# Kernel tuning notes

Hardware: AMD Instinct MI355X
Metric: run time of the kernel (lower is better)

The kernel has to match this reference:

```python
import jax, jax.numpy as jnp
import numpy as np

B, N, COUT, CIN, H, W = 16, 4, 256, 256, 64, 64


def setup_inputs() -> dict:
    key = jax.random.key(0)
    k1, k2, k3, k4 = jax.random.split(key, 4)
    x = jax.random.normal(k1, (B, CIN, H, W), jnp.float32)
    alphas = jax.random.uniform(k2, (B, N), jnp.float32)          # routing weights (lambdas)
    angles = jax.random.normal(k3, (B, N), jnp.float32) * 0.5     # thetas, mixed signs
    # kaiming_normal_(mode='fan_out', relu): std = sqrt(2 / (Cout * k * k))
    std = np.sqrt(2.0 / (COUT * 9)).astype(np.float32)
    weight = jax.random.normal(k4, (N, COUT, CIN, 3, 3), jnp.float32) * std
    return {"x": x, "alphas": alphas, "angles": angles, "weight": weight}


def _rot_mats(thetas):
    """thetas: [M] -> rotation matrices [M, 9, 9] (row, col), matching torch builder."""
    xc = jnp.cos(thetas)
    ys = jnp.sin(thetas)
    a = xc - ys
    b = xc * ys
    c = xc + ys
    z = jnp.zeros_like(xc)
    o = jnp.ones_like(xc)

    def mat(rows):
        # rows: list of 9 lists of 9 [M]-arrays -> [M, 9, 9]
        return jnp.stack([jnp.stack(r, axis=-1) for r in rows], axis=-2)

    pos = mat([
        [a, 1 - a, z, z, z, z, z, z, z],
        [z, xc - b, b, z, 1 - c + b, ys - b, z, z, z],
        [z, z, a, z, z, 1 - a, z, z, z],
        [b, ys - b, z, xc - b, 1 - c + b, z, z, z, z],
        [z, z, z, z, o, z, z, z, z],
        [z, z, z, z, 1 - c + b, xc - b, z, ys - b, b],
        [z, z, z, 1 - a, z, z, a, z, z],
        [z, z, z, ys - b, 1 - c + b, z, b, xc - b, z],
        [z, z, z, z, z, z, z, 1 - a, a],
    ])
    neg = mat([
        [c, z, z, 1 - c, z, z, z, z, z],
        [-b, xc + b, z, b - ys, 1 - a - b, z, z, z, z],
        [z, 1 - c, c, z, z, z, z, z, z],
        [z, z, z, xc + b, 1 - a - b, z, -b, b - ys, z],
        [z, z, z, z, o, z, z, z, z],
        [z, b - ys, -b, z, 1 - a - b, xc + b, z, z, z],
        [z, z, z, z, z, z, c, 1 - c, z],
        [z, z, z, z, 1 - a - b, b - ys, z, xc + b, -b],
        [z, z, z, z, z, 1 - c, z, z, c],
    ])
    m = (thetas >= 0).astype(thetas.dtype)[:, None, None]
    return m * pos + (1 - m) * neg


def reference(x, alphas, angles, weight):
    bsz, Cin, h, w = x.shape
    n, Cout = weight.shape[0], weight.shape[1]
    # [bsz, n, 9, 9] rotation matrices scaled by routing lambdas
    rm = _rot_mats(angles.reshape(-1)).reshape(bsz, n, 9, 9)
    rm = rm * alphas[:, :, None, None]
    # weights [n, Cout, Cin, 3, 3] -> [n, 9, Cout*Cin]
    Wf = weight.transpose(0, 3, 4, 1, 2).reshape(n, 9, Cout * Cin)
    # mix over kernel_number n and source tap q -> per-sample rotated kernels
    rw = jnp.einsum('bnpq,nqm->bpm', rm, Wf)          # [bsz, 9, Cout*Cin]
    rw = rw.reshape(bsz, 3, 3, Cout, Cin).transpose(0, 3, 4, 1, 2)
    rw = rw.reshape(bsz * Cout, Cin, 3, 3)
    # per-sample conv via grouped conv on flattened batch
    xr = x.reshape(1, bsz * Cin, h, w)
    out = jax.lax.conv_general_dilated(
        xr, rw, window_strides=(1, 1), padding=((1, 1), (1, 1)),
        dimension_numbers=('NCHW', 'OIHW', 'NCHW'), feature_group_count=bsz)
    return out.reshape(bsz, Cout, out.shape[2], out.shape[3])
```

## Files before the change

### kernel.cpp

```cpp
#include <hip/hip_runtime.h>
#include <hip/hip_bf16.h>

#define B_    16
#define N_    4
#define COUT  256
#define CIN   256
#define H_    64
#define W_    64
#define K_TOT (CIN * 9)
#define HW    (H_ * W_)
#define NKT   (K_TOT / 32)
#define PAD   66
#define PLANE (PAD * PAD)

typedef __attribute__((ext_vector_type(8))) short short8;
typedef __attribute__((ext_vector_type(4))) float f32x4;
typedef unsigned short ushort_t;

static __device__ __forceinline__ ushort_t f2bf(float f) {
    __hip_bfloat16 h = __float2bfloat16(f);
    return *reinterpret_cast<ushort_t*>(&h);
}

typedef __attribute__((address_space(3))) unsigned int lds_u32;
typedef __attribute__((address_space(1))) const unsigned int glb_u32;
static __device__ __forceinline__ void gl_lds16(const ushort_t* g, ushort_t* l) {
    __builtin_amdgcn_global_load_lds((glb_u32*)g, (lds_u32*)l, 16, 0, 0);
}

#define BARRIER() asm volatile("s_barrier" ::: "memory")
#define VMCNTN(N) asm volatile("s_waitcnt vmcnt(" #N ")" ::: "memory")

__global__ void rot_mats_kernel(const float* __restrict__ alphas,
                                const float* __restrict__ angles,
                                float* __restrict__ rm) {
    int i = threadIdx.x;
    if (i >= B_ * N_) return;
    float th = angles[i], al = alphas[i];
    float xc = cosf(th), ys = sinf(th);
    float a = xc - ys, b = xc * ys, c = xc + ys;
    float r[81];
#pragma unroll
    for (int j = 0; j < 81; ++j) r[j] = 0.f;
    if (th >= 0.f) {
        r[0] = a;          r[1] = 1.f - a;
        r[10] = xc - b;    r[11] = b;        r[13] = 1.f - c + b; r[14] = ys - b;
        r[20] = a;         r[23] = 1.f - a;
        r[27] = b;         r[28] = ys - b;   r[30] = xc - b;      r[31] = 1.f - c + b;
        r[40] = 1.f;
        r[49] = 1.f - c + b; r[50] = xc - b; r[52] = ys - b;      r[53] = b;
        r[57] = 1.f - a;   r[60] = a;
        r[66] = ys - b;    r[67] = 1.f - c + b; r[69] = b;        r[70] = xc - b;
        r[79] = 1.f - a;   r[80] = a;
    } else {
        r[0] = c;          r[3] = 1.f - c;
        r[9] = -b;         r[10] = xc + b;   r[12] = b - ys;      r[13] = 1.f - a - b;
        r[19] = 1.f - c;   r[20] = c;
        r[30] = xc + b;    r[31] = 1.f - a - b; r[33] = -b;       r[34] = b - ys;
        r[40] = 1.f;
        r[46] = b - ys;    r[47] = -b;       r[49] = 1.f - a - b; r[50] = xc + b;
        r[60] = c;         r[61] = 1.f - c;
        r[67] = 1.f - a - b; r[68] = b - ys; r[70] = xc + b;      r[71] = -b;
        r[77] = 1.f - c;   r[80] = c;
    }
#pragma unroll
    for (int j = 0; j < 81; ++j) rm[i * 81 + j] = r[j] * al;
}

__global__ __launch_bounds__(256)
void build_rw_kernel(const float* __restrict__ weight,
                     const float* __restrict__ rm,
                     ushort_t* __restrict__ rw) {
    __shared__ float rms[N_ * 81];
    int tid = threadIdx.x;
    int b = blockIdx.y;
    for (int j = tid; j < N_ * 81; j += 256)
        rms[j] = rm[b * N_ * 81 + j];
    __syncthreads();

    int idx = blockIdx.x * 256 + tid;
    int cout = idx >> 8, cin = idx & 255;

    float wv[N_][9];
#pragma unroll
    for (int n = 0; n < N_; ++n)
#pragma unroll
        for (int q = 0; q < 9; ++q)
            wv[n][q] = weight[(size_t)(n * (COUT * CIN) + idx) * 9 + q];

    ushort_t* dst = rw + (size_t)(b * COUT + cout) * K_TOT + cin;
#pragma unroll
    for (int p = 0; p < 9; ++p) {
        float s = 0.f;
#pragma unroll
        for (int n = 0; n < N_; ++n)
#pragma unroll
            for (int q = 0; q < 9; ++q)
                s += rms[n * 81 + p * 9 + q] * wv[n][q];
        dst[p * 256] = f2bf(s);
    }
}

__global__ __launch_bounds__(256)
void halo_zero_kernel(ushort_t* __restrict__ xt) {
    ushort_t* base = xt + (size_t)blockIdx.x * PLANE * 64;
    int t = threadIdx.x;
    for (int i = t; i < 260; i += 256) {
        int py, px;
        if (i < 66)       { py = 0;  px = i; }
        else if (i < 132) { py = 65; px = i - 66; }
        else if (i < 196) { py = i - 132 + 1; px = 0; }
        else              { py = i - 196 + 1; px = 65; }
        ushort_t* d = base + (size_t)(py * PAD + px) * 64;
        int4 z = {0, 0, 0, 0};
#pragma unroll
        for (int q = 0; q < 8; ++q) *(int4*)(d + q * 8) = z;
    }
}

__global__ __launch_bounds__(256)
void nhwc_kernel(const float* __restrict__ x, ushort_t* __restrict__ xt) {
    int y    = blockIdx.x;
    int cb32 = blockIdx.y;
    int b    = blockIdx.z;
    __shared__ ushort_t tileT[64][40];
    int t = threadIdx.x;

    int ci = t & 31, seg = t >> 5;
    const float* src = x + ((size_t)(b * CIN + cb32 * 32 + ci) * HW + y * 64 + seg * 8);
    float4 f0 = ((const float4*)src)[0];
    float4 f1 = ((const float4*)src)[1];
#pragma unroll
    for (int q = 0; q < 4; ++q) tileT[seg * 8 + q][ci]     = f2bf(((float*)&f0)[q]);
#pragma unroll
    for (int q = 0; q < 4; ++q) tileT[seg * 8 + 4 + q][ci] = f2bf(((float*)&f1)[q]);
    __syncthreads();

    int px = t >> 2, cseg = t & 3;
    ushort_t* dst = xt + ((size_t)(b * 4 + (cb32 >> 1)) * PLANE + (y + 1) * PAD + px + 1) * 64
                       + (cb32 & 1) * 32 + cseg * 8;
    *(int4*)dst = *(const int4*)&tileT[px][cseg * 8];
}

__global__ __launch_bounds__(512, 1)
void conv_kernel(const ushort_t* __restrict__ xt,
                 const ushort_t* __restrict__ rw,
                 float* __restrict__ out) {
    int bid0 = blockIdx.x;
    int bid = (bid0 & 7) * 32 + (bid0 >> 3);
    int b    = bid >> 4;
    int tile = bid & 15;
    int y0 = tile * 4;
    int tid = threadIdx.x;
    int lane = tid & 63, wid = tid >> 6;
    int wm = wid >> 2, wn = wid & 3;
    int rA = lane & 15, kseg = lane >> 4;

    __shared__ __align__(16) ushort_t As[4][256][32];
    __shared__ __align__(16) ushort_t Bs[4][256][32];
    ushort_t* AsB = &As[0][0][0];
    ushort_t* BsB = &Bs[0][0][0];

    f32x4 acc[8][4] = {};

    const ushort_t* rwb  = rw + (size_t)b * COUT * K_TOT;
    const ushort_t* xtb2 = xt + (size_t)b * 4 * PLANE * 64 + (size_t)y0 * PAD * 64;

    const int r0 = tid >> 2;
    const int sd = tid & 3;
    const int fs = (r0 & 3) ^ ((r0 >> 2) & 3);
    const int sg = (sd ^ fs) * 8;
    const int a0 = r0 * K_TOT + sg;
    const int a1 = (r0 + 128) * K_TOT + sg;
    const int pb0 = ((r0 >> 6) * PAD + (r0 & 63)) * 64 + sg;
    const int pb1 = pb0 + 2 * PAD * 64;
    const int dd0 = tid * 8;
    const int dd1 = 4096 + tid * 8;
    const int fread = (rA & 3) ^ ((rA >> 2) & 3);
    const int cread = (kseg ^ fread) * 8;

#define STAGE_A(KTN)                                                           \
    {                                                                          \
        int p_ = (KTN) >> 3, c32_ = (KTN) & 7;                                 \
        int ako = p_ * 256 + c32_ * 32;                                        \
        ushort_t* db = AsB + ((KTN) & 3) * 8192;                               \
        gl_lds16(rwb + a0 + ako, db + dd0);                                    \
        gl_lds16(rwb + a1 + ako, db + dd1);                                    \
    }

#define STAGE_B(KTN)                                                           \
    {                                                                          \
        int p_ = (KTN) >> 3, cb4_ = ((KTN) & 7) >> 1, h_ = (KTN) & 1;          \
        int ph_ = p_ / 3, pw_ = p_ - 3 * ph_;                                  \
        const ushort_t* sb = xtb2 + (size_t)(cb4_ * PLANE + ph_ * PAD + pw_) * 64 \
                             + h_ * 32;                                        \
        ushort_t* db = BsB + ((KTN) & 3) * 8192;                               \
        gl_lds16(sb + pb0, db + dd0);                                          \
        gl_lds16(sb + pb1, db + dd1);                                          \
    }

#define READ_AF(Q, MH2)                                                        \
    _Pragma("unroll")                                                          \
    for (int mi = 0; mi < 4; ++mi) {                                           \
        int row = wm * 128 + (MH2) * 64 + mi * 16 + rA;                        \
        af[mi] = *(const short8*)(AsB + (Q) * 8192 + row * 32 + cread);        \
    }

#define READ_BF(Q)                                                             \
    _Pragma("unroll")                                                          \
    for (int ni = 0; ni < 4; ++ni) {                                           \
        int row = wn * 64 + ni * 16 + rA;                                      \
        bf[ni] = *(const short8*)(BsB + (Q) * 8192 + row * 32 + cread);        \
    }

#define DO_MFMA(MH2)                                                           \
    __builtin_amdgcn_s_setprio(1);                                             \
    _Pragma("unroll")                                                          \
    for (int mi = 0; mi < 4; ++mi)                                             \
        _Pragma("unroll")                                                      \
        for (int ni = 0; ni < 4; ++ni)                                         \
            acc[(MH2) * 4 + mi][ni] = __builtin_amdgcn_mfma_f32_16x16x32_bf16( \
                af[mi], bf[ni], acc[(MH2) * 4 + mi][ni], 0, 0, 0);             \
    __builtin_amdgcn_s_setprio(0);

    STAGE_A(0); STAGE_B(0);
    STAGE_A(1); STAGE_B(1);
    STAGE_A(2); STAGE_B(2);
    VMCNTN(8);
    BARRIER();

    short8 af[4], bf[4];
    for (int kt = 0; kt < NKT; ++kt) {
        int q = kt & 3;
        bool more = (kt + 3 < NKT);
        READ_AF(q, 0);
        READ_BF(q);
        if (more) STAGE_A(kt + 3);
        BARRIER();
        DO_MFMA(0);
        BARRIER();
        READ_AF(q, 1);
        if (more) STAGE_B(kt + 3);
        BARRIER();
        DO_MFMA(1);
        if (kt < NKT - 3)       { VMCNTN(8); }
        else if (kt == NKT - 3) { VMCNTN(4); }
        else if (kt == NKT - 2) { VMCNTN(0); }
        BARRIER();
    }
#undef STAGE_A
#undef STAGE_B
#undef READ_AF
#undef READ_BF
#undef DO_MFMA

    int row0 = (lane >> 4) * 4;
    int col  = lane & 15;
    float* outb = out + (size_t)b * COUT * HW + tile * 256;
#pragma unroll
    for (int am = 0; am < 8; ++am)
#pragma unroll
        for (int an = 0; an < 4; ++an)
#pragma unroll
            for (int rr = 0; rr < 4; ++rr) {
                int m = wm * 128 + am * 16 + row0 + rr;
                int n = wn * 64 + an * 16 + col;
                outb[(size_t)m * HW + n] = acc[am][an][rr];
            }
}

extern "C" void kernel_launch(void* const* d_in, const int* in_sizes, int n_in,
                              void* d_out, int out_size, void* d_ws, size_t ws_size,
                              hipStream_t stream) {
    const float* x      = (const float*)d_in[0];
    const float* alphas = (const float*)d_in[1];
    const float* angles = (const float*)d_in[2];
    const float* weight = (const float*)d_in[3];
    float* out = (float*)d_out;

    ushort_t* rw = (ushort_t*)d_ws;
    ushort_t* xt = (ushort_t*)((char*)d_ws + (size_t)B_ * COUT * K_TOT * 2);
    float*    rm = (float*)((char*)d_ws + (size_t)B_ * COUT * K_TOT * 2
                                        + (size_t)64 * PLANE * 64 * 2);

    rot_mats_kernel<<<1, 64, 0, stream>>>(alphas, angles, rm);
    build_rw_kernel<<<dim3(COUT * CIN / 256, B_), 256, 0, stream>>>(weight, rm, rw);
    halo_zero_kernel<<<64, 256, 0, stream>>>(xt);
    nhwc_kernel<<<dim3(64, 8, B_), 256, 0, stream>>>(x, xt);
    conv_kernel<<<256, 512, 0, stream>>>(xt, rw, out);
}
```

Baseline: 124.6 us.

## Halve conv N-tile to 128 pixels, double K-step to 64, triple-buffer

The conv GEMM tile changes from 256x256 to 256x128 (two output rows per block), which doubles the grid to 512 blocks so more of the CUs are filled. The K step per iteration doubles to 64 with a new XOR swizzle over 8 chunks, and the LDS pipeline moves from four to three stages with A and B staged together. Halving the tile lowers accumulator register pressure and raises parallelism. In exchange, each block reloads the weight tile for half as many pixels, so global and L2 traffic for the A operand roughly doubles.

```diff
diff --git a/kernel.cpp b/kernel.cpp
--- a/kernel.cpp
+++ b/kernel.cpp
@@ -9,7 +9,7 @@
 #define W_    64
 #define K_TOT (CIN * 9)
 #define HW    (H_ * W_)
-#define NKT   (K_TOT / 32)
+#define NKT   (K_TOT / 64)
 #define PAD   66
 #define PLANE (PAD * PAD)
 
@@ -147,70 +147,74 @@
                  const ushort_t* __restrict__ rw,
                  float* __restrict__ out) {
     int bid0 = blockIdx.x;
-    int bid = (bid0 & 7) * 32 + (bid0 >> 3);
-    int b    = bid >> 4;
-    int tile = bid & 15;
-    int y0 = tile * 4;
+    int bid = (bid0 & 7) * 64 + (bid0 >> 3);
+    int b    = bid >> 5;
+    int tile = bid & 31;
+    int y0 = tile * 2;
     int tid = threadIdx.x;
     int lane = tid & 63, wid = tid >> 6;
     int wm = wid >> 2, wn = wid & 3;
     int rA = lane & 15, kseg = lane >> 4;
 
-    __shared__ __align__(16) ushort_t As[4][256][32];
-    __shared__ __align__(16) ushort_t Bs[4][256][32];
+    __shared__ __align__(16) ushort_t As[3][256][64];
+    __shared__ __align__(16) ushort_t Bs[3][128][64];
     ushort_t* AsB = &As[0][0][0];
     ushort_t* BsB = &Bs[0][0][0];
 
-    f32x4 acc[8][4] = {};
+    f32x4 acc[8][2] = {};
 
     const ushort_t* rwb  = rw + (size_t)b * COUT * K_TOT;
     const ushort_t* xtb2 = xt + (size_t)b * 4 * PLANE * 64 + (size_t)y0 * PAD * 64;
 
-    const int r0 = tid >> 2;
-    const int sd = tid & 3;
-    const int fs = (r0 & 3) ^ ((r0 >> 2) & 3);
-    const int sg = (sd ^ fs) * 8;
-    const int a0 = r0 * K_TOT + sg;
-    const int a1 = (r0 + 128) * K_TOT + sg;
-    const int pb0 = ((r0 >> 6) * PAD + (r0 & 63)) * 64 + sg;
-    const int pb1 = pb0 + 2 * PAD * 64;
-    const int dd0 = tid * 8;
-    const int dd1 = 4096 + tid * 8;
-    const int fread = (rA & 3) ^ ((rA >> 2) & 3);
-    const int cread = (kseg ^ fread) * 8;
-
-#define STAGE_A(KTN)                                                           \
+    const int chnk = ((lane & 7) ^ (lane >> 3)) * 8;
+    const int arr  = (lane >> 3);
+    int asrc[4], adst[4];
+#pragma unroll
+    for (int i = 0; i < 4; ++i) {
+        int r = wid * 32 + i * 8 + arr;
+        asrc[i] = r * K_TOT + chnk;
+        adst[i] = ((wid * 4 + i) * 64 + lane) * 8;
+    }
+    int bsrc[2], bdst[2];
+#pragma unroll
+    for (int i = 0; i < 2; ++i) {
+        int r = wid * 16 + i * 8 + arr;
+        bsrc[i] = ((r >> 6) * PAD + (r & 63)) * 64 + chnk;
+        bdst[i] = ((wid * 2 + i) * 64 + lane) * 8;
+    }
+    const int c0 = ((0 + kseg) ^ (rA & 7)) * 8;
+    const int c1 = ((4 + kseg) ^ (rA & 7)) * 8;
+
+#define STAGE(KTN, QS)                                                         \
     {                                                                          \
-        int p_ = (KTN) >> 3, c32_ = (KTN) & 7;                                 \
-        int ako = p_ * 256 + c32_ * 32;                                        \
-        ushort_t* db = AsB + ((KTN) & 3) * 8192;                               \
-        gl_lds16(rwb + a0 + ako, db + dd0);                                    \
-        gl_lds16(rwb + a1 + ako, db + dd1);                                    \
-    }
-
-#define STAGE_B(KTN)                                                           \
-    {                                                                          \
-        int p_ = (KTN) >> 3, cb4_ = ((KTN) & 7) >> 1, h_ = (KTN) & 1;          \
+        int p_ = (KTN) / 4, c4_ = (KTN) & 3;                                   \
+        int ako = p_ * 256 + c4_ * 64;                                         \
         int ph_ = p_ / 3, pw_ = p_ - 3 * ph_;                                  \
-        const ushort_t* sb = xtb2 + (size_t)(cb4_ * PLANE + ph_ * PAD + pw_) * 64 \
-                             + h_ * 32;                                        \
-        ushort_t* db = BsB + ((KTN) & 3) * 8192;                               \
-        gl_lds16(sb + pb0, db + dd0);                                          \
-        gl_lds16(sb + pb1, db + dd1);                                          \
+        ushort_t* da = AsB + (QS) * 16384;                                     \
+        _Pragma("unroll")                                                      \
+        for (int i = 0; i < 4; ++i)                                            \
+            gl_lds16(rwb + asrc[i] + ako, da + adst[i]);                       \
+        const ushort_t* sb = xtb2 + (size_t)(c4_ * PLANE + ph_ * PAD + pw_) * 64; \
+        ushort_t* db = BsB + (QS) * 8192;                                      \
+        _Pragma("unroll")                                                      \
+        for (int i = 0; i < 2; ++i)                                            \
+            gl_lds16(sb + bsrc[i], db + bdst[i]);                              \
     }
 
 #define READ_AF(Q, MH2)                                                        \
     _Pragma("unroll")                                                          \
     for (int mi = 0; mi < 4; ++mi) {                                           \
         int row = wm * 128 + (MH2) * 64 + mi * 16 + rA;                        \
-        af[mi] = *(const short8*)(AsB + (Q) * 8192 + row * 32 + cread);        \
+        af[mi][0] = *(const short8*)(AsB + (Q) * 16384 + row * 64 + c0);       \
+        af[mi][1] = *(const short8*)(AsB + (Q) * 16384 + row * 64 + c1);       \
     }
 
 #define READ_BF(Q)                                                             \
     _Pragma("unroll")                                                          \
-    for (int ni = 0; ni < 4; ++ni) {                                           \
-        int row = wn * 64 + ni * 16 + rA;                                      \
-        bf[ni] = *(const short8*)(BsB + (Q) * 8192 + row * 32 + cread);        \
+    for (int ni = 0; ni < 2; ++ni) {                                           \
+        int row = wn * 32 + ni * 16 + rA;                                      \
+        bf[ni][0] = *(const short8*)(BsB + (Q) * 8192 + row * 64 + c0);        \
+        bf[ni][1] = *(const short8*)(BsB + (Q) * 8192 + row * 64 + c1);        \
     }
 
 #define DO_MFMA(MH2)                                                           \
@@ -218,53 +222,52 @@
     _Pragma("unroll")                                                          \
     for (int mi = 0; mi < 4; ++mi)                                             \
         _Pragma("unroll")                                                      \
-        for (int ni = 0; ni < 4; ++ni)                                         \
-            acc[(MH2) * 4 + mi][ni] = __builtin_amdgcn_mfma_f32_16x16x32_bf16( \
-                af[mi], bf[ni], acc[(MH2) * 4 + mi][ni], 0, 0, 0);             \
+        for (int ni = 0; ni < 2; ++ni)                                         \
+            _Pragma("unroll")                                                  \
+            for (int kh = 0; kh < 2; ++kh)                                     \
+                acc[(MH2) * 4 + mi][ni] = __builtin_amdgcn_mfma_f32_16x16x32_bf16( \
+                    af[mi][kh], bf[ni][kh], acc[(MH2) * 4 + mi][ni], 0, 0, 0); \
     __builtin_amdgcn_s_setprio(0);
 
-    STAGE_A(0); STAGE_B(0);
-    STAGE_A(1); STAGE_B(1);
-    STAGE_A(2); STAGE_B(2);
-    VMCNTN(8);
+    STAGE(0, 0);
+    STAGE(1, 1);
+    VMCNTN(6);
     BARRIER();
 
-    short8 af[4], bf[4];
+    short8 af[4][2], bf[2][2];
+    int qc = 0;
     for (int kt = 0; kt < NKT; ++kt) {
-        int q = kt & 3;
-        bool more = (kt + 3 < NKT);
-        READ_AF(q, 0);
-        READ_BF(q);
-        if (more) STAGE_A(kt + 3);
+        int qs = (qc == 0) ? 2 : qc - 1;
+        READ_AF(qc, 0);
+        READ_BF(qc);
+        if (kt + 2 < NKT) STAGE(kt + 2, qs);
         BARRIER();
         DO_MFMA(0);
         BARRIER();
-        READ_AF(q, 1);
-        if (more) STAGE_B(kt + 3);
+        READ_AF(qc, 1);
         BARRIER();
         DO_MFMA(1);
-        if (kt < NKT - 3)       { VMCNTN(8); }
-        else if (kt == NKT - 3) { VMCNTN(4); }
+        if (kt < NKT - 2)       { VMCNTN(6); }
         else if (kt == NKT - 2) { VMCNTN(0); }
         BARRIER();
-    }
-#undef STAGE_A
-#undef STAGE_B
+        qc = (qc == 2) ? 0 : qc + 1;
+    }
+#undef STAGE
 #undef READ_AF
 #undef READ_BF
 #undef DO_MFMA
 
     int row0 = (lane >> 4) * 4;
     int col  = lane & 15;
-    float* outb = out + (size_t)b * COUT * HW + tile * 256;
+    float* outb = out + (size_t)b * COUT * HW + tile * 128;
 #pragma unroll
     for (int am = 0; am < 8; ++am)
 #pragma unroll
-        for (int an = 0; an < 4; ++an)
+        for (int an = 0; an < 2; ++an)
 #pragma unroll
             for (int rr = 0; rr < 4; ++rr) {
                 int m = wm * 128 + am * 16 + row0 + rr;
-                int n = wn * 64 + an * 16 + col;
+                int n = wn * 32 + an * 16 + col;
                 outb[(size_t)m * HW + n] = acc[am][an][rr];
             }
 }
@@ -287,5 +290,5 @@
     build_rw_kernel<<<dim3(COUT * CIN / 256, B_), 256, 0, stream>>>(weight, rm, rw);
     halo_zero_kernel<<<64, 256, 0, stream>>>(xt);
     nhwc_kernel<<<dim3(64, 8, B_), 256, 0, stream>>>(x, xt);
-    conv_kernel<<<256, 512, 0, stream>>>(xt, rw, out);
-}
+    conv_kernel<<<512, 512, 0, stream>>>(xt, rw, out);
+}
```

New measurement: 141.6 us. 13.6% more time.

## Stage padded input slab in LDS once per channel block, stream weights from global

Applied to the files above, without the earlier changes.

Replaces the 4-stage global_load_lds pipeline for both operands with a double-buffered LDS slab holding the padded 6x66 input rows for 64 channels. The nine 3x3 taps are read as shifted windows of that slab, so each input element is loaded once per channel block instead of once per tap. Weight fragments now go straight from global memory into registers with no LDS staging. Launch bounds request 2 blocks per CU, but the larger per-block LDS footprint and the longer global latency on weight loads may hurt occupancy and latency hiding.

```diff
diff --git a/kernel.cpp b/kernel.cpp
--- a/kernel.cpp
+++ b/kernel.cpp
@@ -9,9 +9,9 @@
 #define W_    64
 #define K_TOT (CIN * 9)
 #define HW    (H_ * W_)
-#define NKT   (K_TOT / 32)
 #define PAD   66
 #define PLANE (PAD * PAD)
+#define SLABU 25344
 
 typedef __attribute__((ext_vector_type(8))) short short8;
 typedef __attribute__((ext_vector_type(4))) float f32x4;
@@ -21,15 +21,6 @@
     __hip_bfloat16 h = __float2bfloat16(f);
     return *reinterpret_cast<ushort_t*>(&h);
 }
-
-typedef __attribute__((address_space(3))) unsigned int lds_u32;
-typedef __attribute__((address_space(1))) const unsigned int glb_u32;
-static __device__ __forceinline__ void gl_lds16(const ushort_t* g, ushort_t* l) {
-    __builtin_amdgcn_global_load_lds((glb_u32*)g, (lds_u32*)l, 16, 0, 0);
-}
-
-#define BARRIER() asm volatile("s_barrier" ::: "memory")
-#define VMCNTN(N) asm volatile("s_waitcnt vmcnt(" #N ")" ::: "memory")
 
 __global__ void rot_mats_kernel(const float* __restrict__ alphas,
                                 const float* __restrict__ angles,
@@ -142,7 +133,7 @@
     *(int4*)dst = *(const int4*)&tileT[px][cseg * 8];
 }
 
-__global__ __launch_bounds__(512, 1)
+__global__ __launch_bounds__(512, 2)
 void conv_kernel(const ushort_t* __restrict__ xt,
                  const ushort_t* __restrict__ rw,
                  float* __restrict__ out) {
@@ -156,103 +147,91 @@
     int wm = wid >> 2, wn = wid & 3;
     int rA = lane & 15, kseg = lane >> 4;
 
-    __shared__ __align__(16) ushort_t As[4][256][32];
-    __shared__ __align__(16) ushort_t Bs[4][256][32];
-    ushort_t* AsB = &As[0][0][0];
-    ushort_t* BsB = &Bs[0][0][0];
+    __shared__ __align__(16) ushort_t slab[2][SLABU];
 
     f32x4 acc[8][4] = {};
 
-    const ushort_t* rwb  = rw + (size_t)b * COUT * K_TOT;
-    const ushort_t* xtb2 = xt + (size_t)b * 4 * PLANE * 64 + (size_t)y0 * PAD * 64;
-
-    const int r0 = tid >> 2;
-    const int sd = tid & 3;
-    const int fs = (r0 & 3) ^ ((r0 >> 2) & 3);
-    const int sg = (sd ^ fs) * 8;
-    const int a0 = r0 * K_TOT + sg;
-    const int a1 = (r0 + 128) * K_TOT + sg;
-    const int pb0 = ((r0 >> 6) * PAD + (r0 & 63)) * 64 + sg;
-    const int pb1 = pb0 + 2 * PAD * 64;
-    const int dd0 = tid * 8;
-    const int dd1 = 4096 + tid * 8;
-    const int fread = (rA & 3) ^ ((rA >> 2) & 3);
-    const int cread = (kseg ^ fread) * 8;
-
-#define STAGE_A(KTN)                                                           \
-    {                                                                          \
-        int p_ = (KTN) >> 3, c32_ = (KTN) & 7;                                 \
-        int ako = p_ * 256 + c32_ * 32;                                        \
-        ushort_t* db = AsB + ((KTN) & 3) * 8192;                               \
-        gl_lds16(rwb + a0 + ako, db + dd0);                                    \
-        gl_lds16(rwb + a1 + ako, db + dd1);                                    \
-    }
-
-#define STAGE_B(KTN)                                                           \
-    {                                                                          \
-        int p_ = (KTN) >> 3, cb4_ = ((KTN) & 7) >> 1, h_ = (KTN) & 1;          \
-        int ph_ = p_ / 3, pw_ = p_ - 3 * ph_;                                  \
-        const ushort_t* sb = xtb2 + (size_t)(cb4_ * PLANE + ph_ * PAD + pw_) * 64 \
-                             + h_ * 32;                                        \
-        ushort_t* db = BsB + ((KTN) & 3) * 8192;                               \
-        gl_lds16(sb + pb0, db + dd0);                                          \
-        gl_lds16(sb + pb1, db + dd1);                                          \
-    }
-
-#define READ_AF(Q, MH2)                                                        \
-    _Pragma("unroll")                                                          \
-    for (int mi = 0; mi < 4; ++mi) {                                           \
-        int row = wm * 128 + (MH2) * 64 + mi * 16 + rA;                        \
-        af[mi] = *(const short8*)(AsB + (Q) * 8192 + row * 32 + cread);        \
-    }
-
-#define READ_BF(Q)                                                             \
-    _Pragma("unroll")                                                          \
-    for (int ni = 0; ni < 4; ++ni) {                                           \
-        int row = wn * 64 + ni * 16 + rA;                                      \
-        bf[ni] = *(const short8*)(BsB + (Q) * 8192 + row * 32 + cread);        \
-    }
-
-#define DO_MFMA(MH2)                                                           \
-    __builtin_amdgcn_s_setprio(1);                                             \
-    _Pragma("unroll")                                                          \
-    for (int mi = 0; mi < 4; ++mi)                                             \
-        _Pragma("unroll")                                                      \
-        for (int ni = 0; ni < 4; ++ni)                                         \
-            acc[(MH2) * 4 + mi][ni] = __builtin_amdgcn_mfma_f32_16x16x32_bf16( \
-                af[mi], bf[ni], acc[(MH2) * 4 + mi][ni], 0, 0, 0);             \
-    __builtin_amdgcn_s_setprio(0);
-
-    STAGE_A(0); STAGE_B(0);
-    STAGE_A(1); STAGE_B(1);
-    STAGE_A(2); STAGE_B(2);
-    VMCNTN(8);
-    BARRIER();
-
-    short8 af[4], bf[4];
-    for (int kt = 0; kt < NKT; ++kt) {
-        int q = kt & 3;
-        bool more = (kt + 3 < NKT);
-        READ_AF(q, 0);
-        READ_BF(q);
-        if (more) STAGE_A(kt + 3);
-        BARRIER();
-        DO_MFMA(0);
-        BARRIER();
-        READ_AF(q, 1);
-        if (more) STAGE_B(kt + 3);
-        BARRIER();
-        DO_MFMA(1);
-        if (kt < NKT - 3)       { VMCNTN(8); }
-        else if (kt == NKT - 3) { VMCNTN(4); }
-        else if (kt == NKT - 2) { VMCNTN(0); }
-        BARRIER();
-    }
-#undef STAGE_A
-#undef STAGE_B
-#undef READ_AF
-#undef READ_BF
-#undef DO_MFMA
+    const ushort_t* rwb = rw + (size_t)b * COUT * K_TOT;
+    const ushort_t* xtb = xt + (size_t)b * 4 * PLANE * 64;
+
+    const ushort_t* aBase = rwb + (size_t)(wm * 128 + rA) * K_TOT + kseg * 8;
+
+    int bpix[4];
+#pragma unroll
+    for (int ni = 0; ni < 4; ++ni) {
+        int pidx = wn * 64 + ni * 16 + rA;
+        bpix[ni] = (pidx >> 6) * PAD + (pidx & 63);
+    }
+
+#define SRC_OFF(U) ((((U) & ~7) + (((U) & 7) ^ (((U) >> 3) & 7))) * 8)
+    const bool tail = tid < 96;
+
+    {
+        const ushort_t* g = xtb + (size_t)y0 * PAD * 64;
+#pragma unroll
+        for (int ps = 0; ps < 6; ++ps) {
+            int u = ps * 512 + tid;
+            short8 v = *(const short8*)(g + SRC_OFF(u));
+            *(short8*)(&slab[0][u * 8]) = v;
+        }
+        if (tail) {
+            int u = 3072 + tid;
+            short8 v = *(const short8*)(g + SRC_OFF(u));
+            *(short8*)(&slab[0][u * 8]) = v;
+        }
+    }
+    __syncthreads();
+
+    int buf = 0;
+    for (int cb4 = 0; cb4 < 4; ++cb4) {
+        const ushort_t* gnext = xtb + (size_t)((cb4 + 1) * PLANE + y0 * PAD) * 64;
+        const ushort_t* ab4 = aBase + cb4 * 64;
+        const ushort_t* sl = &slab[buf][0];
+        ushort_t* sln = &slab[buf ^ 1][0];
+        bool more = (cb4 < 3);
+
+#pragma unroll
+        for (int p = 0; p < 9; ++p) {
+            const int ph = p / 3, pw = p - 3 * ph;
+            if (more) {
+                if (p < 6) {
+                    int u = p * 512 + tid;
+                    short8 v = *(const short8*)(gnext + SRC_OFF(u));
+                    *(short8*)(&sln[u * 8]) = v;
+                } else if (p == 6 && tail) {
+                    int u = 3072 + tid;
+                    short8 v = *(const short8*)(gnext + SRC_OFF(u));
+                    *(short8*)(&sln[u * 8]) = v;
+                }
+            }
+            const ushort_t* ab = ab4 + p * 256;
+#pragma unroll
+            for (int kh = 0; kh < 2; ++kh) {
+                short8 a[8];
+#pragma unroll
+                for (int mi = 0; mi < 8; ++mi)
+                    a[mi] = *(const short8*)(ab + (size_t)mi * 16 * K_TOT + kh * 32);
+                short8 bv[4];
+#pragma unroll
+                for (int ni = 0; ni < 4; ++ni) {
+                    int rs = bpix[ni] + ph * PAD + pw;
+                    bv[ni] = *(const short8*)(&sl[rs * 64
+                              + ((((kh << 2) | kseg) ^ (rs & 7)) * 8)]);
+                }
+                __builtin_amdgcn_s_setprio(1);
+#pragma unroll
+                for (int mi = 0; mi < 8; ++mi)
+#pragma unroll
+                    for (int ni = 0; ni < 4; ++ni)
+                        acc[mi][ni] = __builtin_amdgcn_mfma_f32_16x16x32_bf16(
+                            a[mi], bv[ni], acc[mi][ni], 0, 0, 0);
+                __builtin_amdgcn_s_setprio(0);
+            }
+        }
+        __syncthreads();
+        buf ^= 1;
+    }
+#undef SRC_OFF
 
     int row0 = (lane >> 4) * 4;
     int col  = lane & 15;
```

Result: slower. 218.8 us (+75.6%).
